# Performance work log

Measured on AMD Instinct MI355X. Metric: run time of the kernel, lower is better.

## Reference

```python
import jax, jax.numpy as jnp
import numpy as np
from jax import lax

SCALE = 4
PATCH = 3
CR = 2
SOFTMAX_FACTOR = 10.0
B, H, W, C = 8, 64, 64, 64
CI = C // CR


def prelu(x, alpha):
    return jnp.where(x >= 0, x, alpha * x)


def conv1x1(x, w, b):
    return jnp.einsum('bhwc,cd->bhwd', x, w) + b


def _same_pad(in_size, k, s):
    out = -(-in_size // s)
    pad = max((out - 1) * s + k - in_size, 0)
    return pad // 2, pad - pad // 2, out


def extract_patches(x, k, s):
    # x: [B,H,W,C] -> [B, outH, outW, k, k, C], SAME zero padding (TF extract_patches)
    b, h, w, c = x.shape
    plh, phh, oh = _same_pad(h, k, s)
    plw, phw, ow = _same_pad(w, k, s)
    xp = jnp.pad(x, ((0, 0), (plh, phh), (plw, phw), (0, 0)))
    rows = (jnp.arange(oh) * s)[:, None] + jnp.arange(k)[None, :]  # [oh,k]
    cols = (jnp.arange(ow) * s)[:, None] + jnp.arange(k)[None, :]  # [ow,k]
    p = xp[:, rows]              # [B, oh, k, Wp, C]
    p = p[:, :, :, cols]         # [B, oh, k, ow, k, C]
    return p.transpose(0, 1, 3, 2, 4, 5)


def setup_inputs() -> dict:
    key = jax.random.key(0)
    ks = jax.random.split(key, 8)
    def glorot(k, shape):
        fan_in, fan_out = shape[0], shape[1]
        std = np.sqrt(2.0 / (fan_in + fan_out))
        return jax.random.normal(k, shape, dtype=jnp.float32) * std
    return {
        'x': jax.random.normal(ks[0], (B, H, W, C), dtype=jnp.float32),
        'theta_w': glorot(ks[1], (C, CI)),
        'theta_b': jnp.zeros((CI,), jnp.float32),
        'theta_alpha': jax.random.uniform(ks[2], (CI,), jnp.float32, 0.0, 0.3),
        'phi_w': glorot(ks[3], (C, CI)),
        'phi_b': jnp.zeros((CI,), jnp.float32),
        'phi_alpha': jax.random.uniform(ks[4], (CI,), jnp.float32, 0.0, 0.3),
        'g_w': glorot(ks[5], (C, C)),
        'g_b': jnp.zeros((C,), jnp.float32),
        'g_alpha': jax.random.uniform(ks[6], (C,), jnp.float32, 0.0, 0.3),
    }


def reference(x, theta_w, theta_b, theta_alpha, phi_w, phi_b, phi_alpha, g_w, g_b, g_alpha):
    b, h, w, c = x.shape
    s, p = SCALE, PATCH
    hs, ws = h // s, w // s
    n = hs * ws
    sp = s * p
    ci = c // CR

    theta = prelu(conv1x1(x, theta_w, theta_b), theta_alpha)                  # [B,H,W,Ci]
    phi_in = jax.image.resize(x, (b, hs, ws, c), method='bilinear', antialias=False)
    phi = prelu(conv1x1(phi_in, phi_w, phi_b), phi_alpha)                     # [B,Hs,Ws,Ci]
    phi_patch = extract_patches(phi, p, 1).reshape(b, n, p, p, ci)            # [B,N,3,3,Ci]
    g = prelu(conv1x1(x, g_w, g_b), g_alpha)                                  # [B,H,W,C]
    g_patch = extract_patches(g, sp, s).reshape(b, n, sp, sp, c)              # [B,N,12,12,C]

    # L2-normalize each phi patch (per patch, over kh,kw,ci)
    norm = jnp.sqrt(jnp.sum(phi_patch * phi_patch, axis=(2, 3, 4), keepdims=True))
    phi_n = phi_patch / jnp.maximum(norm, 1e-6)

    # patch matching == SAME 3x3 correlation of theta with N dynamic filters
    theta_patch = extract_patches(theta, p, 1)                                # [B,H,W,3,3,Ci]
    scores = jnp.einsum('bhwpqc,bnpqc->bhwn', theta_patch, phi_n)             # [B,H,W,N]
    attn = jax.nn.softmax(scores * SOFTMAX_FACTOR, axis=-1)

    # conv2d_transpose with per-sample filters [sp,sp,C,N], stride s, SAME
    pad_lo, pad_hi, _ = _same_pad(s * h, sp, s)  # forward-conv SAME pads (4,4)
    pads = (sp - 1 - pad_lo, sp - 1 - pad_hi)

    def deconv(y_i, g_i):
        # y_i: [H,W,N]; g_i: [N,sp,sp,C]
        ker = g_i.transpose(1, 2, 0, 3)[::-1, ::-1]  # spatially flipped, HWIO (I=N,O=C)
        out = lax.conv_general_dilated(
            y_i[None], ker, window_strides=(1, 1),
            padding=[pads, pads], lhs_dilation=(s, s),
            dimension_numbers=('NHWC', 'HWIO', 'NHWC'))
        return out[0]

    y = jax.vmap(deconv)(attn, g_patch)  # [B, s*H, s*W, C]
    return y / 6.0
```

## Files before the change

### kernel.cpp

```cpp
#include <hip/hip_runtime.h>
#include <math.h>

#define BB 8

typedef __attribute__((ext_vector_type(8))) short short8;
typedef __attribute__((ext_vector_type(4))) float f32x4;

__device__ inline short f2bf(float x) {
  unsigned u = __builtin_bit_cast(unsigned, x);
  u += 0x7fffu + ((u >> 16) & 1u);
  return (short)(u >> 16);
}
__device__ inline float bf2f(short h) {
  unsigned u = ((unsigned)(unsigned short)h) << 16;
  return __builtin_bit_cast(float, u);
}

__device__ inline void gload_lds16(const void* g, void* l) {
  __builtin_amdgcn_global_load_lds(
      (const __attribute__((address_space(1))) void*)g,
      (__attribute__((address_space(3))) void*)l, 16, 0, 0);
}

__device__ inline void ring_px(int p, int& r, int& cc) {
  if (p < 66) { r = 0; cc = p; }
  else if (p < 132) { r = 65; cc = p - 66; }
  else { int q = p - 132; r = 1 + (q >> 1); cc = (q & 1) ? 65 : 0; }
}

__global__ __launch_bounds__(256) void k_pre(const float* __restrict__ x,
                          const float* __restrict__ theta_w, const float* __restrict__ theta_b,
                          const float* __restrict__ theta_alpha,
                          const float* __restrict__ phi_w, const float* __restrict__ phi_b,
                          const float* __restrict__ phi_alpha,
                          const float* __restrict__ g_w, const float* __restrict__ g_b,
                          const float* __restrict__ g_alpha,
                          short* __restrict__ thetaPh, short* __restrict__ thetaPl,
                          short* __restrict__ gOut,
                          short* __restrict__ Bh, short* __restrict__ Bl) {
  __shared__ __align__(16) float spool[14528];
  int tid = threadIdx.x;
  if (blockIdx.x < 256) {
    int bid = blockIdx.x;
    int b = bid >> 5, pg = bid & 31;
    int px0 = pg * 128;
    if (tid <= 32) {
      int c = pg + 32 * tid;
      if (c < 1040) {
        int p = c >> 2, off = (c & 3) * 8;
        int r, cc; ring_px(p, r, cc);
        size_t ad = ((size_t)(b * 66 + r) * 66 + cc) * 32 + off;
        short8 z = (short8)0;
        *(short8*)(thetaPh + ad) = z;
        *(short8*)(thetaPl + ad) = z;
      }
    }
    float* gw = spool;
    float* tw = spool + 4096;
    float* xs = spool + 6144;
    float* gb_s = spool + 14336; float* ga_s = spool + 14400;
    float* tb_s = spool + 14464; float* ta_s = spool + 14496;
    for (int idx = tid; idx < 1024; idx += 256) ((float4*)gw)[idx] = ((const float4*)g_w)[idx];
    for (int idx = tid; idx < 512; idx += 256)  ((float4*)tw)[idx] = ((const float4*)theta_w)[idx];
    if (tid < 64) { gb_s[tid] = g_b[tid]; ga_s[tid] = g_alpha[tid]; }
    else if (tid < 96) { tb_s[tid - 64] = theta_b[tid - 64]; ta_s[tid - 64] = theta_alpha[tid - 64]; }
    {
      int p = tid >> 1, half = tid & 1;
      const float* xp = x + ((size_t)b * 4096 + px0 + p) * 64 + half * 32;
      #pragma unroll
      for (int i = 0; i < 8; ++i) {
        float4 v = ((const float4*)xp)[i];
        int k = half * 32 + i * 4;
        xs[(k + 0) * 128 + p] = v.x; xs[(k + 1) * 128 + p] = v.y;
        xs[(k + 2) * 128 + p] = v.z; xs[(k + 3) * 128 + p] = v.w;
      }
    }
    __syncthreads();
    int pp = tid >> 2, q = tid & 3;
    float accg[2][16], acct[2][8];
    #pragma unroll
    for (int c = 0; c < 16; ++c) { float bv = gb_s[q * 16 + c]; accg[0][c] = bv; accg[1][c] = bv; }
    #pragma unroll
    for (int c = 0; c < 8; ++c)  { float bv = tb_s[q * 8 + c];  acct[0][c] = bv; acct[1][c] = bv; }
    for (int k = 0; k < 64; ++k) {
      float x0 = xs[k * 128 + 2 * pp], x1 = xs[k * 128 + 2 * pp + 1];
      const float* gwr = gw + k * 64 + q * 16;
      const float* twr = tw + k * 32 + q * 8;
      #pragma unroll
      for (int c = 0; c < 16; ++c) { float wv = gwr[c]; accg[0][c] += x0 * wv; accg[1][c] += x1 * wv; }
      #pragma unroll
      for (int c = 0; c < 8; ++c)  { float wv = twr[c]; acct[0][c] += x0 * wv; acct[1][c] += x1 * wv; }
    }
    #pragma unroll
    for (int e = 0; e < 2; ++e) {
      int px = px0 + 2 * pp + e;
      short* gp = gOut + ((size_t)(b * 4096 + px)) * 64 + q * 16;
      short8 gv0, gv1;
      #pragma unroll
      for (int c = 0; c < 16; ++c) {
        float v = accg[e][c];
        float a = ga_s[q * 16 + c];
        v = v >= 0.f ? v : a * v;
        short hb = f2bf(v);
        if (c < 8) gv0[c] = hb; else gv1[c - 8] = hb;
      }
      *(short8*)(gp) = gv0;
      *(short8*)(gp + 8) = gv1;
      int h = px >> 6, w = px & 63;
      size_t off = ((size_t)(b * 66 + h + 1) * 66 + (w + 1)) * 32 + q * 8;
      short8 hv, lv;
      #pragma unroll
      for (int c = 0; c < 8; ++c) {
        float t = acct[e][c];
        float a = ta_s[q * 8 + c];
        float v = t >= 0.f ? t : a * t;
        short hi = f2bf(v);
        hv[c] = hi;
        lv[c] = f2bf(v - bf2f(hi));
      }
      *(short8*)(thetaPh + off) = hv;
      *(short8*)(thetaPl + off) = lv;
    }
  } else {
    int bid = blockIdx.x - 256;
    int b = bid >> 4, irow = bid & 15;
    float* pw   = spool;
    float* pb   = spool + 2048;
    float* pa   = spool + 2080;
    float* ph_s = spool + 2112;
    float* ss2  = spool + 3696;
    float* ssp  = spool + 3744;
    for (int idx = tid; idx < 512; idx += 256) ((float4*)pw)[idx] = ((const float4*)phi_w)[idx];
    if (tid < 32) { pb[tid] = phi_b[tid]; pa[tid] = phi_alpha[tid]; }
    __syncthreads();
    if (tid < 192) {
      int lr = tid >> 6, j = (tid >> 2) & 15, cg = tid & 3;
      int i2 = irow + lr - 1;
      float acc8[8];
      float sum2 = 0.f;
      if (i2 >= 0 && i2 < 16) {
        #pragma unroll
        for (int c = 0; c < 8; ++c) acc8[c] = pb[cg * 8 + c];
        const float* xb = x + (size_t)b * 4096 * 64;
        const float* p00 = xb + ((size_t)(4 * i2 + 1) * 64 + (4 * j + 1)) * 64;
        for (int kq = 0; kq < 16; ++kq) {
          float4 a = ((const float4*)p00)[kq];
          float4 bq = ((const float4*)(p00 + 64))[kq];
          float4 cq = ((const float4*)(p00 + 4096))[kq];
          float4 dq = ((const float4*)(p00 + 4160))[kq];
          float xv[4] = {0.25f * (a.x + bq.x + cq.x + dq.x), 0.25f * (a.y + bq.y + cq.y + dq.y),
                         0.25f * (a.z + bq.z + cq.z + dq.z), 0.25f * (a.w + bq.w + cq.w + dq.w)};
          #pragma unroll
          for (int e = 0; e < 4; ++e) {
            const float* pwr = pw + (kq * 4 + e) * 32 + cg * 8;
            #pragma unroll
            for (int c = 0; c < 8; ++c) acc8[c] += xv[e] * pwr[c];
          }
        }
        #pragma unroll
        for (int c = 0; c < 8; ++c) {
          float v = acc8[c];
          v = v >= 0.f ? v : pa[cg * 8 + c] * v;
          ph_s[(lr * 16 + j) * 33 + cg * 8 + c] = v;
          sum2 += v * v;
        }
      } else {
        #pragma unroll
        for (int c = 0; c < 8; ++c) ph_s[(lr * 16 + j) * 33 + cg * 8 + c] = 0.f;
      }
      ssp[tid] = sum2;
    }
    __syncthreads();
    if (tid < 48) ss2[tid] = ssp[tid*4] + ssp[tid*4+1] + ssp[tid*4+2] + ssp[tid*4+3];
    __syncthreads();
    int j = tid >> 4, u = tid & 15;
    if (u < 9) {
      float nn = 0.f;
      #pragma unroll
      for (int lr = 0; lr < 3; ++lr) {
        int i2 = irow + lr - 1;
        if (i2 < 0 || i2 > 15) continue;
        #pragma unroll
        for (int dj = 0; dj < 3; ++dj) {
          int pj = j + dj - 1;
          if (pj >= 0 && pj < 16) nn += ss2[lr * 16 + pj];
        }
      }
      float scale = 1.f / fmaxf(sqrtf(nn), 1e-6f);
      int lr = u / 3, dj = u % 3;
      int i2 = irow + lr - 1, pj = j + dj - 1;
      bool ok = (i2 >= 0 && i2 < 16 && pj >= 0 && pj < 16);
      size_t base = ((size_t)(b * 256 + irow * 16 + j)) * 288 + u * 32;
      #pragma unroll
      for (int q8 = 0; q8 < 4; ++q8) {
        short8 hv, lv;
        #pragma unroll
        for (int c = 0; c < 8; ++c) {
          float v = ok ? ph_s[(lr * 16 + pj) * 33 + q8 * 8 + c] * scale : 0.f;
          short hi = f2bf(v);
          hv[c] = hi;
          lv[c] = f2bf(v - bf2f(hi));
        }
        *(short8*)(Bh + base + q8 * 8) = hv;
        *(short8*)(Bl + base + q8 * 8) = lv;
      }
    }
  }
}

__global__ __launch_bounds__(256) void k_bgather(const short* __restrict__ g,
                                                 short* __restrict__ Bbf) {
  int r = blockIdx.x;
  int bl = blockIdx.y;
  int ry = r >> 2, rx = r & 3;
  int t = threadIdx.x;
  int wv = t >> 6, l = t & 63;
  int jj = t >> 4, c4 = (t & 15) * 4;
  __shared__ short tile[256 * 66];
  const short* gb = g + (size_t)bl * 4096 * 64;
  for (int s = 0; s < 9; ++s) {
    int dy = s / 3, dx = s % 3;
    {
      int col = 4 * jj + rx + 4 * dx - 4;
      #pragma unroll
      for (int i2 = 0; i2 < 16; ++i2) {
        int row = 4 * i2 + ry + 4 * dy - 4;
        short4 v = make_short4(0, 0, 0, 0);
        if (row >= 0 && row < 64 && col >= 0 && col < 64)
          v = *(const short4*)(gb + (((size_t)row << 6) + col) * 64 + c4);
        int ij = i2 * 16 + jj;
        tile[ij * 66 + c4 + 0] = v.x;
        tile[ij * 66 + c4 + 1] = v.y;
        tile[ij * 66 + c4 + 2] = v.z;
        tile[ij * 66 + c4 + 3] = v.w;
      }
    }
    __syncthreads();
    #pragma unroll
    for (int cc = 0; cc < 16; ++cc) {
      int c = cc * 4 + wv;
      int n = r * 64 + c;
      unsigned* dstrow = (unsigned*)(Bbf + ((size_t)bl * 1024 + n) * 2304 + s * 256);
      #pragma unroll
      for (int half = 0; half < 2; ++half) {
        int ij0 = half * 128 + 2 * l;
        unsigned v = (unsigned)(unsigned short)tile[ij0 * 66 + c]
                   | ((unsigned)(unsigned short)tile[(ij0 + 1) * 66 + c] << 16);
        dstrow[half * 64 + l] = v;
      }
    }
    __syncthreads();
  }
}

__global__ __launch_bounds__(512) void k_mid(const short* __restrict__ g,
                                             short* __restrict__ Bbf,
                                             const short* __restrict__ thetaPh,
                                             const short* __restrict__ thetaPl,
                                             const short* __restrict__ Bh,
                                             const short* __restrict__ Bl,
                                             short* __restrict__ attnp,
                                             int doGather) {
  __shared__ __align__(16) short smem[32768];
  int tid = threadIdx.x;
  int b = blockIdx.y;
  if (blockIdx.x < 16) {
    if (!doGather) return;
    int r = blockIdx.x, bl = b;
    int ry = r >> 2, rx = r & 3;
    short* tile = smem;
    const short* gb = g + (size_t)bl * 4096 * 64;
    for (int s = 0; s < 9; ++s) {
      int dy = s / 3, dx = s % 3;
      if (tid < 256) {
        int jj = tid >> 4, c4 = (tid & 15) * 4;
        int col = 4 * jj + rx + 4 * dx - 4;
        #pragma unroll
        for (int i2 = 0; i2 < 16; ++i2) {
          int row = 4 * i2 + ry + 4 * dy - 4;
          short4 v = make_short4(0, 0, 0, 0);
          if (row >= 0 && row < 64 && col >= 0 && col < 64)
            v = *(const short4*)(gb + (((size_t)row << 6) + col) * 64 + c4);
          int ij = i2 * 16 + jj;
          tile[ij * 66 + c4 + 0] = v.x;
          tile[ij * 66 + c4 + 1] = v.y;
          tile[ij * 66 + c4 + 2] = v.z;
          tile[ij * 66 + c4 + 3] = v.w;
        }
      }
      __syncthreads();
      if (tid < 256) {
        int wv = tid >> 6, l = tid & 63;
        #pragma unroll
        for (int cc = 0; cc < 16; ++cc) {
          int c = cc * 4 + wv;
          int n = r * 64 + c;
          unsigned* dstrow = (unsigned*)(Bbf + ((size_t)bl * 1024 + n) * 2304 + s * 256);
          #pragma unroll
          for (int half = 0; half < 2; ++half) {
            int ij0 = half * 128 + 2 * l;
            unsigned v = (unsigned)(unsigned short)tile[ij0 * 66 + c]
                       | ((unsigned)(unsigned short)tile[(ij0 + 1) * 66 + c] << 16);
            dstrow[half * 64 + l] = v;
          }
        }
      }
      __syncthreads();
    }
    return;
  }
  int mt = blockIdx.x - 16;
  {
    int c = mt + 32 * tid;
    if (c < 8320) {
      int p = c >> 5, off = (c & 31) * 8;
      int r, cc; ring_px(p, r, cc);
      *(short8*)(attnp + ((size_t)(b * 66 + r) * 66 + cc) * 256 + off) = (short8)0;
    }
  }
  int w = tid >> 6, lane = tid & 63;
  int wm = w >> 2, wn = w & 3;
  int quad = lane >> 4, l16 = lane & 15;

  short* Ash = smem;
  short* Asl = smem + 4096;
  short* Bsh = smem + 8192;
  short* Bsl = smem + 16384;
  float* wred = (float*)(smem + 24576);

  f32x4 acc[4][4];
  #pragma unroll
  for (int i = 0; i < 4; ++i)
    #pragma unroll
    for (int j = 0; j < 4; ++j) acc[i][j] = (f32x4)0.f;

  int ar = w * 16 + (lane >> 2);
  int am = mt * 128 + ar;
  int aQy = am >> 6, aQx = am & 63;
  int achunk = (lane & 3) * 8;

  for (int s = 0; s < 9; ++s) {
    int di = s / 3, dj = s % 3;
    __syncthreads();
    size_t aoff = ((size_t)(b * 66 + aQy + di) * 66 + (aQx + dj)) * 32 + achunk;
    gload_lds16(thetaPh + aoff, Ash + w * 512 + lane * 8);
    gload_lds16(thetaPl + aoff, Asl + w * 512 + lane * 8);
    #pragma unroll
    for (int p = 0; p < 2; ++p) {
      int nl = w * 32 + p * 16 + (lane >> 2);
      size_t boff = ((size_t)(b * 256 + nl)) * 288 + s * 32 + achunk;
      gload_lds16(Bh + boff, Bsh + w * 1024 + p * 512 + lane * 8);
      gload_lds16(Bl + boff, Bsl + w * 1024 + p * 512 + lane * 8);
    }
    __syncthreads();
    #pragma unroll
    for (int pass = 0; pass < 3; ++pass) {
      const short* Asrc = (pass < 2) ? Ash : Asl;
      const short* Bsrc = (pass == 1) ? Bsl : Bsh;
      short8 af[4], bfr[4];
      #pragma unroll
      for (int i = 0; i < 4; ++i)
        af[i] = *(const short8*)(Asrc + (wm * 64 + i * 16 + l16) * 32 + quad * 8);
      #pragma unroll
      for (int j = 0; j < 4; ++j)
        bfr[j] = *(const short8*)(Bsrc + (wn * 64 + j * 16 + l16) * 32 + quad * 8);
      #pragma unroll
      for (int i = 0; i < 4; ++i)
        #pragma unroll
        for (int j = 0; j < 4; ++j)
          acc[i][j] = __builtin_amdgcn_mfma_f32_16x16x32_bf16(af[i], bfr[j], acc[i][j], 0, 0, 0);
    }
  }

  float rmax[4][4];
  #pragma unroll
  for (int i = 0; i < 4; ++i)
    #pragma unroll
    for (int reg = 0; reg < 4; ++reg) {
      float m = -1e30f;
      #pragma unroll
      for (int j = 0; j < 4; ++j) m = fmaxf(m, acc[i][j][reg]);
      #pragma unroll
      for (int off = 1; off < 16; off <<= 1) m = fmaxf(m, __shfl_xor(m, off));
      rmax[i][reg] = m;
    }
  if (l16 == 0) {
    #pragma unroll
    for (int i = 0; i < 4; ++i)
      #pragma unroll
      for (int reg = 0; reg < 4; ++reg)
        wred[(wm * 64 + i * 16 + quad * 4 + reg) * 4 + wn] = rmax[i][reg];
  }
  __syncthreads();
  #pragma unroll
  for (int i = 0; i < 4; ++i)
    #pragma unroll
    for (int reg = 0; reg < 4; ++reg) {
      int r = wm * 64 + i * 16 + quad * 4 + reg;
      rmax[i][reg] = fmaxf(fmaxf(wred[r * 4 + 0], wred[r * 4 + 1]),
                           fmaxf(wred[r * 4 + 2], wred[r * 4 + 3]));
    }
  __syncthreads();
  float rsum[4][4];
  #pragma unroll
  for (int i = 0; i < 4; ++i)
    #pragma unroll
    for (int reg = 0; reg < 4; ++reg) {
      float s = 0.f;
      #pragma unroll
      for (int j = 0; j < 4; ++j) {
        float e = expf((acc[i][j][reg] - rmax[i][reg]) * 10.f);
        acc[i][j][reg] = e;
        s += e;
      }
      #pragma unroll
      for (int off = 1; off < 16; off <<= 1) s += __shfl_xor(s, off);
      rsum[i][reg] = s;
    }
  if (l16 == 0) {
    #pragma unroll
    for (int i = 0; i < 4; ++i)
      #pragma unroll
      for (int reg = 0; reg < 4; ++reg)
        wred[(wm * 64 + i * 16 + quad * 4 + reg) * 4 + wn] = rsum[i][reg];
  }
  __syncthreads();
  #pragma unroll
  for (int i = 0; i < 4; ++i)
    #pragma unroll
    for (int reg = 0; reg < 4; ++reg) {
      int r = wm * 64 + i * 16 + quad * 4 + reg;
      float tot = wred[r * 4 + 0] + wred[r * 4 + 1] + wred[r * 4 + 2] + wred[r * 4 + 3];
      rsum[i][reg] = 1.f / tot;
    }
  __syncthreads();
  #pragma unroll
  for (int i = 0; i < 4; ++i)
    #pragma unroll
    for (int reg = 0; reg < 4; ++reg) {
      int r = wm * 64 + i * 16 + quad * 4 + reg;
      #pragma unroll
      for (int j = 0; j < 4; ++j)
        smem[r * 256 + wn * 64 + j * 16 + l16] = f2bf(acc[i][j][reg] * rsum[i][reg]);
    }
  __syncthreads();
  {
    int r2 = tid >> 2, c2 = (tid & 3) * 64;
    int m2 = mt * 128 + r2;
    int Qy = m2 >> 6, Qx = m2 & 63;
    short8* dst = (short8*)(attnp + ((size_t)(b * 66 + Qy + 1) * 66 + (Qx + 1)) * 256 + c2);
    #pragma unroll
    for (int q = 0; q < 8; ++q) dst[q] = *(const short8*)(smem + r2 * 256 + c2 + q * 8);
  }
}

__global__ __launch_bounds__(256) void k_gemm(const short* __restrict__ attnp,
                                              const short* __restrict__ Bbf,
                                              float* __restrict__ out,
                                              int b0) {
  int lid = blockIdx.x + 32 * blockIdx.y + 256 * blockIdx.z;
  int nwg = 256 * gridDim.z;
  int chunk = nwg >> 3;
  int swz = (lid & 7) * chunk + (lid >> 3);
  int mt = swz & 31;
  int nt = (swz >> 5) & 7;
  int bl = swz >> 8;
  int b = b0 + bl;
  int tid = threadIdx.x;
  int wave = tid >> 6, lane = tid & 63;
  int wm = wave >> 1, wn = wave & 1;
  int quad = lane >> 4, l16 = lane & 15;

  __shared__ __align__(16) short As[12288];
  __shared__ __align__(16) short Bs[12288];

  f32x4 acc[4][4];
  #pragma unroll
  for (int i = 0; i < 4; ++i)
    #pragma unroll
    for (int j = 0; j < 4; ++j) acc[i][j] = (f32x4)0.f;

  const short* Ab = attnp + (size_t)b * 66 * 66 * 256;
  const short* Bb = Bbf + (size_t)bl * 1024 * 2304 + (size_t)(nt * 128) * 2304;

  int larow = lane >> 2;
  int cl8 = ((lane & 3) ^ ((lane >> 3) & 3)) * 8;

  int rr0 = wave * 32 + larow, rr1 = rr0 + 16;
  int m0 = mt * 128 + rr0,     m1 = mt * 128 + rr1;
  const short* aB0 = Ab + ((size_t)(((m0 >> 6) + 2) * 66 + (m0 & 63) + 2) << 8) + cl8;
  const short* aB1 = Ab + ((size_t)(((m1 >> 6) + 2) * 66 + (m1 & 63) + 2) << 8) + cl8;
  const short* bB0 = Bb + (size_t)rr0 * 2304 + cl8;
  const short* bB1 = Bb + (size_t)rr1 * 2304 + cl8;

  int po = (quad ^ ((l16 >> 1) & 3)) * 8;

  for (int kb0 = 0; kb0 < 24; ++kb0) {
    __syncthreads();
    #pragma unroll
    for (int u = 0; u < 3; ++u) {
      int kb = kb0 * 3 + u;
      int s = kb >> 3;
      int dy = (s * 11) >> 5;
      int dx = s - 3 * dy;
      int offA = (kb & 7) * 32 - ((dy * 66 + dx) << 8);
      int offB = kb * 32;
      gload_lds16(aB0 + offA, As + u * 4096 + wave * 1024 + lane * 8);
      gload_lds16(bB0 + offB, Bs + u * 4096 + wave * 1024 + lane * 8);
      gload_lds16(aB1 + offA, As + u * 4096 + wave * 1024 + 512 + lane * 8);
      gload_lds16(bB1 + offB, Bs + u * 4096 + wave * 1024 + 512 + lane * 8);
    }
    __syncthreads();
    #pragma unroll
    for (int u = 0; u < 3; ++u) {
      short8 af[4], bfr[4];
      #pragma unroll
      for (int i = 0; i < 4; ++i)
        af[i] = *(const short8*)(As + u * 4096 + (wm * 64 + i * 16 + l16) * 32 + po);
      #pragma unroll
      for (int j = 0; j < 4; ++j)
        bfr[j] = *(const short8*)(Bs + u * 4096 + (wn * 64 + j * 16 + l16) * 32 + po);
      #pragma unroll
      for (int i = 0; i < 4; ++i)
        #pragma unroll
        for (int j = 0; j < 4; ++j)
          acc[i][j] = __builtin_amdgcn_mfma_f32_16x16x32_bf16(af[i], bfr[j], acc[i][j], 0, 0, 0);
    }
  }

  const float inv6 = 1.f / 6.f;
  #pragma unroll
  for (int i = 0; i < 4; ++i) {
    int mbase = mt * 128 + wm * 64 + i * 16 + quad * 4;
    #pragma unroll
    for (int j = 0; j < 4; ++j) {
      int n = nt * 128 + wn * 64 + j * 16 + l16;
      int r = n >> 6; int c = n & 63;
      int ry = r >> 2, rx = r & 3;
      #pragma unroll
      for (int reg = 0; reg < 4; ++reg) {
        int m = mbase + reg;
        int Qy = m >> 6, Qx = m & 63;
        out[(((size_t)b * 256 + 4 * Qy + ry) * 256 + (4 * Qx + rx)) * 64 + c]
            = acc[i][j][reg] * inv6;
      }
    }
  }
}

extern "C" void kernel_launch(void* const* d_in, const int* in_sizes, int n_in,
                              void* d_out, int out_size, void* d_ws, size_t ws_size,
                              hipStream_t stream) {
  const float* x           = (const float*)d_in[0];
  const float* theta_w     = (const float*)d_in[1];
  const float* theta_b     = (const float*)d_in[2];
  const float* theta_alpha = (const float*)d_in[3];
  const float* phi_w       = (const float*)d_in[4];
  const float* phi_b       = (const float*)d_in[5];
  const float* phi_alpha   = (const float*)d_in[6];
  const float* g_w         = (const float*)d_in[7];
  const float* g_b         = (const float*)d_in[8];
  const float* g_alpha     = (const float*)d_in[9];
  float* out = (float*)d_out;

  char* w = (char*)d_ws;
  size_t off = 0;
  auto alloc = [&](size_t bytes) { void* p = w + off; off += (bytes + 255) & ~255ull; return p; };
  short* g       = (short*)alloc(8ull * 4096 * 64 * 2);
  size_t thp_bytes = 8ull * 66 * 66 * 32 * 2;
  short* thetaPh = (short*)alloc(thp_bytes);
  short* thetaPl = (short*)alloc(thp_bytes);
  short* Bh      = (short*)alloc(8ull * 256 * 288 * 2);
  short* Bl      = (short*)alloc(8ull * 256 * 288 * 2);
  size_t attnp_bytes = 8ull * 66 * 66 * 256 * 2;
  short* attnp   = (short*)alloc(attnp_bytes);
  size_t bbf_full = 8ull * 1024 * 2304 * 2;
  bool full = (off + bbf_full) <= ws_size;
  short* Bbf = (short*)alloc(full ? bbf_full : bbf_full / 8);

  hipLaunchKernelGGL(k_pre, dim3(256 + 128), dim3(256), 0, stream,
                     x, theta_w, theta_b, theta_alpha, phi_w, phi_b, phi_alpha,
                     g_w, g_b, g_alpha, thetaPh, thetaPl, g, Bh, Bl);
  if (full) {
    hipLaunchKernelGGL(k_mid, dim3(48, BB), dim3(512), 0, stream,
                       g, Bbf, thetaPh, thetaPl, Bh, Bl, attnp, 1);
    hipLaunchKernelGGL(k_gemm, dim3(32, 8, BB), dim3(256), 0, stream, attnp, Bbf, out, 0);
  } else {
    hipLaunchKernelGGL(k_mid, dim3(48, BB), dim3(512), 0, stream,
                       g, Bbf, thetaPh, thetaPl, Bh, Bl, attnp, 0);
    for (int b = 0; b < BB; ++b) {
      hipLaunchKernelGGL(k_bgather, dim3(16, 1), dim3(256), 0, stream,
                         g + (size_t)b * 4096 * 64, Bbf);
      hipLaunchKernelGGL(k_gemm, dim3(32, 8, 1), dim3(256), 0, stream, attnp, Bbf, out, b);
    }
  }
}
```

Baseline: 387.6 us.

## Software-pipeline GEMM k-loop with 4-deep LDS ring buffer and async loads

```diff
diff --git a/kernel.cpp b/kernel.cpp
--- a/kernel.cpp
+++ b/kernel.cpp
@@ -471,8 +471,8 @@
   int wm = wave >> 1, wn = wave & 1;
   int quad = lane >> 4, l16 = lane & 15;
 
-  __shared__ __align__(16) short As[12288];
-  __shared__ __align__(16) short Bs[12288];
+  __shared__ __align__(16) short As[16384];
+  __shared__ __align__(16) short Bs[16384];
 
   f32x4 acc[4][4];
   #pragma unroll
@@ -494,39 +494,67 @@
   const short* bB1 = Bb + (size_t)rr1 * 2304 + cl8;
 
   int po = (quad ^ ((l16 >> 1) & 3)) * 8;
-
-  for (int kb0 = 0; kb0 < 24; ++kb0) {
-    __syncthreads();
-    #pragma unroll
-    for (int u = 0; u < 3; ++u) {
-      int kb = kb0 * 3 + u;
-      int s = kb >> 3;
-      int dy = (s * 11) >> 5;
-      int dx = s - 3 * dy;
-      int offA = (kb & 7) * 32 - ((dy * 66 + dx) << 8);
-      int offB = kb * 32;
-      gload_lds16(aB0 + offA, As + u * 4096 + wave * 1024 + lane * 8);
-      gload_lds16(bB0 + offB, Bs + u * 4096 + wave * 1024 + lane * 8);
-      gload_lds16(aB1 + offA, As + u * 4096 + wave * 1024 + 512 + lane * 8);
-      gload_lds16(bB1 + offB, Bs + u * 4096 + wave * 1024 + 512 + lane * 8);
-    }
-    __syncthreads();
-    #pragma unroll
-    for (int u = 0; u < 3; ++u) {
-      short8 af[4], bfr[4];
-      #pragma unroll
-      for (int i = 0; i < 4; ++i)
-        af[i] = *(const short8*)(As + u * 4096 + (wm * 64 + i * 16 + l16) * 32 + po);
-      #pragma unroll
-      for (int j = 0; j < 4; ++j)
-        bfr[j] = *(const short8*)(Bs + u * 4096 + (wn * 64 + j * 16 + l16) * 32 + po);
-      #pragma unroll
-      for (int i = 0; i < 4; ++i)
-        #pragma unroll
-        for (int j = 0; j < 4; ++j)
-          acc[i][j] = __builtin_amdgcn_mfma_f32_16x16x32_bf16(af[i], bfr[j], acc[i][j], 0, 0, 0);
-    }
-  }
+  int ldst = wave * 1024 + lane * 8;
+
+  #define STAGE32(kb, bf)                                                       \
+    {                                                                           \
+      int s_ = (kb) >> 3;                                                       \
+      int dy_ = (s_ * 11) >> 5;                                                 \
+      int dx_ = s_ - 3 * dy_;                                                   \
+      int offA_ = ((kb) & 7) * 32 - ((dy_ * 66 + dx_) << 8);                    \
+      int offB_ = (kb) * 32;                                                    \
+      short* la_ = As + (bf) * 4096 + ldst;                                     \
+      short* lb_ = Bs + (bf) * 4096 + ldst;                                     \
+      gload_lds16(aB0 + offA_, la_);                                            \
+      gload_lds16(bB0 + offB_, lb_);                                            \
+      gload_lds16(aB1 + offA_, la_ + 512);                                      \
+      gload_lds16(bB1 + offB_, lb_ + 512);                                      \
+    }
+
+  #define COMPUTE32(c)                                                          \
+    {                                                                           \
+      const short* As_ = As + ((c) & 3) * 4096;                                 \
+      const short* Bs_ = Bs + ((c) & 3) * 4096;                                 \
+      short8 af[4], bfr[4];                                                     \
+      _Pragma("unroll")                                                         \
+      for (int i = 0; i < 4; ++i)                                               \
+        af[i] = *(const short8*)(As_ + (wm * 64 + i * 16 + l16) * 32 + po);     \
+      _Pragma("unroll")                                                         \
+      for (int j = 0; j < 4; ++j)                                               \
+        bfr[j] = *(const short8*)(Bs_ + (wn * 64 + j * 16 + l16) * 32 + po);    \
+      _Pragma("unroll")                                                         \
+      for (int i = 0; i < 4; ++i)                                               \
+        _Pragma("unroll")                                                       \
+        for (int j = 0; j < 4; ++j)                                             \
+          acc[i][j] = __builtin_amdgcn_mfma_f32_16x16x32_bf16(af[i], bfr[j],    \
+                                                              acc[i][j], 0, 0, 0); \
+    }
+
+  STAGE32(0, 0);
+  STAGE32(1, 1);
+  STAGE32(2, 2);
+
+  for (int c = 0; c < 69; ++c) {
+    asm volatile("s_waitcnt vmcnt(8) lgkmcnt(0)" ::: "memory");
+    __builtin_amdgcn_s_barrier();
+    __builtin_amdgcn_sched_barrier(0);
+    STAGE32(c + 3, (c + 3) & 3);
+    COMPUTE32(c);
+  }
+  asm volatile("s_waitcnt vmcnt(8) lgkmcnt(0)" ::: "memory");
+  __builtin_amdgcn_s_barrier();
+  __builtin_amdgcn_sched_barrier(0);
+  COMPUTE32(69);
+  asm volatile("s_waitcnt vmcnt(4) lgkmcnt(0)" ::: "memory");
+  __builtin_amdgcn_s_barrier();
+  __builtin_amdgcn_sched_barrier(0);
+  COMPUTE32(70);
+  asm volatile("s_waitcnt vmcnt(0) lgkmcnt(0)" ::: "memory");
+  __builtin_amdgcn_s_barrier();
+  __builtin_amdgcn_sched_barrier(0);
+  COMPUTE32(71);
+  #undef STAGE32
+  #undef COMPUTE32
 
   const float inv6 = 1.f / 6.f;
   #pragma unroll
```

After: 414.7 us. 1.07x slower.
